# Kernel tuning notes

Measured on AMD Instinct MI355X. Metric: run time of the kernel, lower is better.

The kernel has to match this reference:

```python
import jax, jax.numpy as jnp
import numpy as np


def _bilinear_resize_nchw(x, out_h, out_w):
    """Torch F.interpolate(mode='bilinear', align_corners=False), no antialias."""
    B, C, H, W = x.shape

    def coords(out_n, in_n):
        src = jnp.maximum(0.0, (jnp.arange(out_n, dtype=jnp.float32) + 0.5) * (in_n / out_n) - 0.5)
        f = jnp.floor(src)
        i0 = jnp.clip(f.astype(jnp.int32), 0, in_n - 1)
        i1 = jnp.clip(i0 + 1, 0, in_n - 1)
        frac = src - f
        return i0, i1, frac

    y0, y1, fy = coords(out_h, H)
    x0, x1, fx = coords(out_w, W)
    rows = x[:, :, y0, :] * (1.0 - fy)[None, None, :, None] + x[:, :, y1, :] * fy[None, None, :, None]
    out = rows[:, :, :, x0] * (1.0 - fx)[None, None, None, :] + rows[:, :, :, x1] * fx[None, None, None, :]
    return out


def setup_inputs() -> dict:
    key = jax.random.key(0)
    k1, k2, k3, k4 = jax.random.split(key, 4)
    return {
        "query_value": jax.random.normal(k1, (2, 256, 64, 128), dtype=jnp.float32),
        "memory_keys_low": jax.random.normal(k2, (2, 4, 64, 32, 64), dtype=jnp.float32),
        "memory_values_low": jax.random.normal(k3, (2, 4, 256, 32, 64), dtype=jnp.float32),
        "query_key_low": jax.random.normal(k4, (2, 64, 32, 64), dtype=jnp.float32),
    }


def reference(query_value, memory_keys_low, memory_values_low, query_key_low):
    B, T, Ck, H, W = memory_keys_low.shape
    Cv = memory_values_low.shape[2]
    # keys: BxTxCkxHxW -> Bx(T*H*W)xCk via permute(0,2,1,3,4)+view+permute
    mk = jnp.transpose(memory_keys_low, (0, 2, 1, 3, 4)).reshape(B, Ck, T * H * W)
    qk = query_key_low.reshape(B, Ck, H * W)
    # attn[b, m, n] over memory locations m (softmax axis), query locations n
    attn = jnp.einsum('bcm,bcn->bmn', mk, qk)  # [B, T*H*W, H*W]
    # matmul_norm=False: no key_channels**-0.5 scaling
    attn = jax.nn.softmax(attn, axis=1)
    mv = jnp.transpose(memory_values_low, (0, 2, 1, 3, 4)).reshape(B, Cv, T * H * W)
    memory = jnp.einsum('bcm,bmn->bcn', mv, attn).reshape(B, Cv, H, W)
    qv = _bilinear_resize_nchw(query_value, H, W)
    return jnp.concatenate([qv, memory], axis=1)  # [B, 2*Cv, H, W]
```

## Files before the change

### kernel.cpp

```cpp
#include <hip/hip_runtime.h>
#include <cstdint>

#define BATCH 2
#define TT    4
#define CKD   64
#define CVD   256
#define NQ    2048
#define MM    8192
#define TQ    64
#define TM    32
#define MSPLIT 8
#define MCHUNK (MM / MSPLIT)
#define NIT    (MCHUNK / TM)

typedef unsigned short u16;
typedef __bf16 bf16x8 __attribute__((ext_vector_type(8)));
typedef float  f32x4  __attribute__((ext_vector_type(4)));

struct __attribute__((aligned(8)))  U16x4 { u16 x, y, z, w; };
struct __attribute__((aligned(16))) U16x8 { u16 v[8]; };

__device__ __forceinline__ u16 f2bf(float x) {
    uint32_t u = __float_as_uint(x);
    uint32_t r = (u + 0x7FFFu + ((u >> 16) & 1u)) >> 16;
    return (u16)r;
}
__device__ __forceinline__ float bf2f(u16 h) {
    return __uint_as_float(((uint32_t)h) << 16);
}

#define MFMA(a, b, c) __builtin_amdgcn_mfma_f32_16x16x32_bf16((a), (b), (c), 0, 0, 0)

#define WS_VB   0u
#define WS_KHI  8388608u
#define WS_KLO  10485760u
#define WS_QHI  12582912u
#define WS_QLO  13107200u
#define WS_LP   13631488u
#define WS_UP   13893632u

__global__ __launch_bounds__(256)
void prep_fused(const float* __restrict__ qv, const float* __restrict__ mk,
                const float* __restrict__ qk, const float* __restrict__ mv,
                float* __restrict__ out, u16* __restrict__ vb,
                u16* __restrict__ khi, u16* __restrict__ klo,
                u16* __restrict__ qhi, u16* __restrict__ qlo) {
    __shared__ float tile[64 * 65];
    const int bid = blockIdx.x;
    const int tid = threadIdx.x;

    if (bid < 4096) {
        int idx = bid * 256 + tid;
        int n  = idx & 2047;
        int bc = idx >> 11;
        int x = n & 63, y = n >> 6;
        const float* ib = qv + (size_t)bc * (64 * 128) + (2 * y) * 128 + 2 * x;
        float2 r0 = *(const float2*)ib;
        float2 r1 = *(const float2*)(ib + 128);
        int b = bc >> 8, c = bc & 255;
        out[((size_t)(b * 512 + c)) * NQ + n] = 0.25f * (r0.x + r0.y + r1.x + r1.y);
    } else if (bid < 6144) {
        int idx = (bid - 4096) * 256 + tid;
        const float4* s = (const float4*)mv + (size_t)idx * 2;
        float4 a = s[0], b = s[1];
        U16x8 o;
        o.v[0] = f2bf(a.x); o.v[1] = f2bf(a.y); o.v[2] = f2bf(a.z); o.v[3] = f2bf(a.w);
        o.v[4] = f2bf(b.x); o.v[5] = f2bf(b.y); o.v[6] = f2bf(b.z); o.v[7] = f2bf(b.w);
        *(U16x8*)(vb + (size_t)idx * 8) = o;
    } else {
        const float* src;
        u16 *dhi, *dlo;
        int blk;
        if (bid < 6400) { src = mk; dhi = khi; dlo = klo; blk = bid - 6144; }
        else            { src = qk; dhi = qhi; dlo = qlo; blk = bid - 6400; }
        const int g  = blk >> 5;
        const int mg = blk & 31;
        const float* s = src + (size_t)g * 64 * 2048 + mg * 64;

        const int c = tid >> 2;
        const int q = tid & 3;
        #pragma unroll
        for (int i = 0; i < 4; ++i) {
            float4 v = *(const float4*)(s + (size_t)c * 2048 + q * 16 + i * 4);
            int m = q * 16 + i * 4;
            tile[(m + 0) * 65 + c] = v.x;
            tile[(m + 1) * 65 + c] = v.y;
            tile[(m + 2) * 65 + c] = v.z;
            tile[(m + 3) * 65 + c] = v.w;
        }
        __syncthreads();

        const int mo = tid >> 2;
        const int cb = (tid & 3) * 16;
        U16x8 h0, h1, l0, l1;
        #pragma unroll
        for (int j = 0; j < 8; ++j) {
            float v = tile[mo * 65 + cb + j];
            u16 h = f2bf(v);
            h0.v[j] = h; l0.v[j] = f2bf(v - bf2f(h));
            float v2 = tile[mo * 65 + cb + 8 + j];
            u16 h2 = f2bf(v2);
            h1.v[j] = h2; l1.v[j] = f2bf(v2 - bf2f(h2));
        }
        size_t o = ((size_t)g * 2048 + mg * 64 + mo) * 64 + cb;
        *(U16x8*)(dhi + o) = h0; *(U16x8*)(dhi + o + 8) = h1;
        *(U16x8*)(dlo + o) = l0; *(U16x8*)(dlo + o + 8) = l1;
    }
}

__global__ __launch_bounds__(256, 2)
void flash_attn(const u16* __restrict__ khi_g, const u16* __restrict__ klo_g,
                const u16* __restrict__ vb_g, const u16* __restrict__ qhi_g,
                const u16* __restrict__ qlo_g, float* __restrict__ Up,
                float* __restrict__ Lp) {
    __shared__ __align__(16) u16 smem[2][7168];

    const int tid    = threadIdx.x;
    const int bx     = blockIdx.x;
    const int mchunk = bx & 7;
    const int ntile  = (bx >> 3) & 31;
    const int b      = bx >> 8;

    const int lane = tid & 63;
    const int w    = tid >> 6;
    const int quad = lane >> 4;
    const int l15  = lane & 15;

    const int bt      = b * TT + (mchunk >> 1);
    const int hw_base = (mchunk & 1) * MCHUNK;

    bf16x8 qh[2][2], ql[2][2];
    {
        const int nbase = ntile * TQ + (w >> 1) * 32;
        #pragma unroll
        for (int nsi = 0; nsi < 2; ++nsi) {
            size_t o = ((size_t)(b * NQ + nbase + nsi * 16 + l15)) * 64 + quad * 8;
            qh[nsi][0] = *(const bf16x8*)&qhi_g[o];
            qh[nsi][1] = *(const bf16x8*)&qhi_g[o + 32];
            ql[nsi][0] = *(const bf16x8*)&qlo_g[o];
            ql[nsi][1] = *(const bf16x8*)&qlo_g[o + 32];
        }
    }

    const u16* kh_base = khi_g + ((size_t)bt * 2048 + hw_base) * 64;
    const u16* kl_base = klo_g + ((size_t)bt * 2048 + hw_base) * 64;
    const u16* v_frag_base = vb_g + (size_t)bt * CVD * 2048 + hw_base
                           + (size_t)(w * 64 + l15) * 2048 + quad * 8;

    f32x4 O[4][4];
    #pragma unroll
    for (int i = 0; i < 4; ++i)
        #pragma unroll
        for (int j = 0; j < 4; ++j)
            O[i][j] = (f32x4){0.f, 0.f, 0.f, 0.f};
    float Lloc[2] = {0.f, 0.f};

    const int msub     = w & 1;
    const int nsubpair = w >> 1;

    const int km = tid >> 3;
    const int kc = (tid & 7) * 8;

    bf16x8 kh_r = *(const bf16x8*)&kh_base[(size_t)km * 64 + kc];
    bf16x8 kl_r = *(const bf16x8*)&kl_base[(size_t)km * 64 + kc];
    bf16x8 v_cur[4], v_next[4];
    #pragma unroll
    for (int cs = 0; cs < 4; ++cs)
        v_cur[cs] = *(const bf16x8*)&v_frag_base[(size_t)(cs * 16) * 2048];

    #pragma unroll 2
    for (int it = 0; it < NIT; ++it) {
        u16* Khi = smem[it & 1];
        u16* Klo = Khi + 2304;
        u16* Ps  = Khi + 4608;

        *(bf16x8*)&Khi[km * 72 + kc] = kh_r;
        *(bf16x8*)&Klo[km * 72 + kc] = kl_r;
        __syncthreads();

        f32x4 acc[2];
        acc[0] = (f32x4){0.f, 0.f, 0.f, 0.f};
        acc[1] = (f32x4){0.f, 0.f, 0.f, 0.f};
        #pragma unroll
        for (int ks = 0; ks < 2; ++ks) {
            bf16x8 ah = *(const bf16x8*)&Khi[(msub * 16 + l15) * 72 + ks * 32 + quad * 8];
            bf16x8 al = *(const bf16x8*)&Klo[(msub * 16 + l15) * 72 + ks * 32 + quad * 8];
            #pragma unroll
            for (int nsi = 0; nsi < 2; ++nsi) {
                acc[nsi] = MFMA(ah, qh[nsi][ks], acc[nsi]);
                acc[nsi] = MFMA(ah, ql[nsi][ks], acc[nsi]);
                acc[nsi] = MFMA(al, qh[nsi][ks], acc[nsi]);
            }
        }
        #pragma unroll
        for (int nsi = 0; nsi < 2; ++nsi) {
            int n = (nsubpair * 2 + nsi) * 16 + l15;
            float p0 = __expf(acc[nsi][0]);
            float p1 = __expf(acc[nsi][1]);
            float p2 = __expf(acc[nsi][2]);
            float p3 = __expf(acc[nsi][3]);
            Lloc[nsi] += (p0 + p1) + (p2 + p3);
            U16x4 pk = {f2bf(p0), f2bf(p1), f2bf(p2), f2bf(p3)};
            *(U16x4*)&Ps[n * 40 + msub * 16 + quad * 4] = pk;
        }
        __syncthreads();

        if (it + 1 < NIT) {
            const int hw1 = (it + 1) * TM;
            kh_r = *(const bf16x8*)&kh_base[(size_t)(hw1 + km) * 64 + kc];
            kl_r = *(const bf16x8*)&kl_base[(size_t)(hw1 + km) * 64 + kc];
            #pragma unroll
            for (int cs = 0; cs < 4; ++cs)
                v_next[cs] = *(const bf16x8*)&v_frag_base[(size_t)(cs * 16) * 2048 + hw1];
        }

        bf16x8 a2[4];
        #pragma unroll
        for (int nsub = 0; nsub < 4; ++nsub)
            a2[nsub] = *(const bf16x8*)&Ps[(nsub * 16 + l15) * 40 + quad * 8];
        #pragma unroll
        for (int cs = 0; cs < 4; ++cs)
            #pragma unroll
            for (int nsub = 0; nsub < 4; ++nsub)
                O[nsub][cs] = MFMA(a2[nsub], v_cur[cs], O[nsub][cs]);

        #pragma unroll
        for (int cs = 0; cs < 4; ++cs)
            v_cur[cs] = v_next[cs];
    }

    #pragma unroll
    for (int nsi = 0; nsi < 2; ++nsi) {
        float v = Lloc[nsi];
        v += __shfl_xor(v, 16);
        v += __shfl_xor(v, 32);
        if (quad == nsi) {
            int nsub = nsubpair * 2 + nsi;
            Lp[(((size_t)mchunk * 2 + msub) * BATCH + b) * NQ + ntile * TQ + nsub * 16 + l15] = v;
        }
    }

    float* ubase = Up + (((size_t)mchunk * BATCH + b) * NQ + ntile * TQ) * CVD + w * 64;
    #pragma unroll
    for (int nsub = 0; nsub < 4; ++nsub) {
        #pragma unroll
        for (int cs = 0; cs < 4; ++cs) {
            #pragma unroll
            for (int r = 0; r < 4; ++r) {
                int n_local = nsub * 16 + quad * 4 + r;
                ubase[(size_t)n_local * CVD + cs * 16 + l15] = O[nsub][cs][r];
            }
        }
    }
}

__global__ __launch_bounds__(256) void reduce_div(const float* __restrict__ Up,
                                                  const float* __restrict__ Lp,
                                                  float* __restrict__ out) {
    __shared__ float lds[16 * 65];
    const int tid = threadIdx.x;
    const int cq  = blockIdx.x & 3;
    const int n0  = ((blockIdx.x >> 2) & 127) * 16;
    const int b   = blockIdx.x >> 9;

    const int n_local = tid >> 4;
    const int c_loc   = (tid & 15) * 4;
    const int c       = cq * 64 + c_loc;

    float4 acc = {0.f, 0.f, 0.f, 0.f};
    for (int ms = 0; ms < MSPLIT; ++ms) {
        float4 v = *(const float4*)(Up + (((size_t)ms * BATCH + b) * NQ + n0 + n_local) * CVD + c);
        acc.x += v.x; acc.y += v.y; acc.z += v.z; acc.w += v.w;
    }

    float Lsum = 0.f;
    #pragma unroll
    for (int s = 0; s < MSPLIT * 2; ++s)
        Lsum += Lp[((size_t)s * BATCH + b) * NQ + n0 + n_local];
    const float inv = 1.0f / Lsum;

    lds[n_local * 65 + c_loc + 0] = acc.x * inv;
    lds[n_local * 65 + c_loc + 1] = acc.y * inv;
    lds[n_local * 65 + c_loc + 2] = acc.z * inv;
    lds[n_local * 65 + c_loc + 3] = acc.w * inv;
    __syncthreads();

    const int c_out = tid >> 2;
    const int nq    = (tid & 3) * 4;
    float4 v;
    v.x = lds[(nq + 0) * 65 + c_out];
    v.y = lds[(nq + 1) * 65 + c_out];
    v.z = lds[(nq + 2) * 65 + c_out];
    v.w = lds[(nq + 3) * 65 + c_out];
    *(float4*)(out + ((size_t)(b * 512 + 256 + cq * 64 + c_out)) * NQ + n0 + nq) = v;
}

extern "C" void kernel_launch(void* const* d_in, const int* in_sizes, int n_in,
                              void* d_out, int out_size, void* d_ws, size_t ws_size,
                              hipStream_t stream) {
    const float* qv = (const float*)d_in[0];
    const float* mk = (const float*)d_in[1];
    const float* mv = (const float*)d_in[2];
    const float* qk = (const float*)d_in[3];
    float* out = (float*)d_out;

    u16*   vb  = (u16*)((char*)d_ws + WS_VB);
    u16*   khi = (u16*)((char*)d_ws + WS_KHI);
    u16*   klo = (u16*)((char*)d_ws + WS_KLO);
    u16*   qhi = (u16*)((char*)d_ws + WS_QHI);
    u16*   qlo = (u16*)((char*)d_ws + WS_QLO);
    float* Lp  = (float*)((char*)d_ws + WS_LP);
    float* Up  = (float*)((char*)d_ws + WS_UP);

    prep_fused<<<6464, 256, 0, stream>>>(qv, mk, qk, mv, out, vb, khi, klo, qhi, qlo);
    flash_attn<<<512, 256, 0, stream>>>(khi, klo, vb, qhi, qlo, Up, Lp);
    reduce_div<<<1024, 256, 0, stream>>>(Up, Lp, out);
}
```

Before: 134.6 us.

## Double the memory tile to 64 and give each wave a full query slice

```diff
diff --git a/kernel.cpp b/kernel.cpp
--- a/kernel.cpp
+++ b/kernel.cpp
@@ -8,7 +8,7 @@
 #define NQ    2048
 #define MM    8192
 #define TQ    64
-#define TM    32
+#define TM    64
 #define MSPLIT 8
 #define MCHUNK (MM / MSPLIT)
 #define NIT    (MCHUNK / TM)
@@ -113,7 +113,7 @@
                 const u16* __restrict__ vb_g, const u16* __restrict__ qhi_g,
                 const u16* __restrict__ qlo_g, float* __restrict__ Up,
                 float* __restrict__ Lp) {
-    __shared__ __align__(16) u16 smem[2][7168];
+    __shared__ __align__(16) u16 smem[2][13824];
 
     const int tid    = threadIdx.x;
     const int bx     = blockIdx.x;
@@ -129,17 +129,13 @@
     const int bt      = b * TT + (mchunk >> 1);
     const int hw_base = (mchunk & 1) * MCHUNK;
 
-    bf16x8 qh[2][2], ql[2][2];
+    bf16x8 qh[2], ql[2];
     {
-        const int nbase = ntile * TQ + (w >> 1) * 32;
-        #pragma unroll
-        for (int nsi = 0; nsi < 2; ++nsi) {
-            size_t o = ((size_t)(b * NQ + nbase + nsi * 16 + l15)) * 64 + quad * 8;
-            qh[nsi][0] = *(const bf16x8*)&qhi_g[o];
-            qh[nsi][1] = *(const bf16x8*)&qhi_g[o + 32];
-            ql[nsi][0] = *(const bf16x8*)&qlo_g[o];
-            ql[nsi][1] = *(const bf16x8*)&qlo_g[o + 32];
-        }
+        size_t o = ((size_t)(b * NQ + ntile * TQ + w * 16 + l15)) * 64 + quad * 8;
+        qh[0] = *(const bf16x8*)&qhi_g[o];
+        qh[1] = *(const bf16x8*)&qhi_g[o + 32];
+        ql[0] = *(const bf16x8*)&qlo_g[o];
+        ql[1] = *(const bf16x8*)&qlo_g[o + 32];
     }
 
     const u16* kh_base = khi_g + ((size_t)bt * 2048 + hw_base) * 64;
@@ -153,91 +149,98 @@
         #pragma unroll
         for (int j = 0; j < 4; ++j)
             O[i][j] = (f32x4){0.f, 0.f, 0.f, 0.f};
-    float Lloc[2] = {0.f, 0.f};
-
-    const int msub     = w & 1;
-    const int nsubpair = w >> 1;
-
-    const int km = tid >> 3;
-    const int kc = (tid & 7) * 8;
-
-    bf16x8 kh_r = *(const bf16x8*)&kh_base[(size_t)km * 64 + kc];
-    bf16x8 kl_r = *(const bf16x8*)&kl_base[(size_t)km * 64 + kc];
-    bf16x8 v_cur[4], v_next[4];
+    float Lloc = 0.f;
+
+    const int km = tid >> 2;
+    const int kc = (tid & 3) * 16;
+
+    bf16x8 kh_r0 = *(const bf16x8*)&kh_base[(size_t)km * 64 + kc];
+    bf16x8 kh_r1 = *(const bf16x8*)&kh_base[(size_t)km * 64 + kc + 8];
+    bf16x8 kl_r0 = *(const bf16x8*)&kl_base[(size_t)km * 64 + kc];
+    bf16x8 kl_r1 = *(const bf16x8*)&kl_base[(size_t)km * 64 + kc + 8];
+    bf16x8 v_cur[4][2], v_next[4][2];
     #pragma unroll
     for (int cs = 0; cs < 4; ++cs)
-        v_cur[cs] = *(const bf16x8*)&v_frag_base[(size_t)(cs * 16) * 2048];
+        #pragma unroll
+        for (int ks = 0; ks < 2; ++ks)
+            v_cur[cs][ks] = *(const bf16x8*)&v_frag_base[(size_t)(cs * 16) * 2048 + ks * 32];
 
     #pragma unroll 2
     for (int it = 0; it < NIT; ++it) {
         u16* Khi = smem[it & 1];
-        u16* Klo = Khi + 2304;
-        u16* Ps  = Khi + 4608;
-
-        *(bf16x8*)&Khi[km * 72 + kc] = kh_r;
-        *(bf16x8*)&Klo[km * 72 + kc] = kl_r;
+        u16* Klo = Khi + 4608;
+        u16* Ps  = Khi + 9216;
+
+        *(bf16x8*)&Khi[km * 72 + kc]     = kh_r0;
+        *(bf16x8*)&Khi[km * 72 + kc + 8] = kh_r1;
+        *(bf16x8*)&Klo[km * 72 + kc]     = kl_r0;
+        *(bf16x8*)&Klo[km * 72 + kc + 8] = kl_r1;
         __syncthreads();
 
-        f32x4 acc[2];
-        acc[0] = (f32x4){0.f, 0.f, 0.f, 0.f};
-        acc[1] = (f32x4){0.f, 0.f, 0.f, 0.f};
+        f32x4 acc[4];
+        #pragma unroll
+        for (int ms = 0; ms < 4; ++ms)
+            acc[ms] = (f32x4){0.f, 0.f, 0.f, 0.f};
         #pragma unroll
         for (int ks = 0; ks < 2; ++ks) {
-            bf16x8 ah = *(const bf16x8*)&Khi[(msub * 16 + l15) * 72 + ks * 32 + quad * 8];
-            bf16x8 al = *(const bf16x8*)&Klo[(msub * 16 + l15) * 72 + ks * 32 + quad * 8];
             #pragma unroll
-            for (int nsi = 0; nsi < 2; ++nsi) {
-                acc[nsi] = MFMA(ah, qh[nsi][ks], acc[nsi]);
-                acc[nsi] = MFMA(ah, ql[nsi][ks], acc[nsi]);
-                acc[nsi] = MFMA(al, qh[nsi][ks], acc[nsi]);
+            for (int ms = 0; ms < 4; ++ms) {
+                bf16x8 ah = *(const bf16x8*)&Khi[(ms * 16 + l15) * 72 + ks * 32 + quad * 8];
+                bf16x8 al = *(const bf16x8*)&Klo[(ms * 16 + l15) * 72 + ks * 32 + quad * 8];
+                acc[ms] = MFMA(ah, qh[ks], acc[ms]);
+                acc[ms] = MFMA(ah, ql[ks], acc[ms]);
+                acc[ms] = MFMA(al, qh[ks], acc[ms]);
             }
         }
         #pragma unroll
-        for (int nsi = 0; nsi < 2; ++nsi) {
-            int n = (nsubpair * 2 + nsi) * 16 + l15;
-            float p0 = __expf(acc[nsi][0]);
-            float p1 = __expf(acc[nsi][1]);
-            float p2 = __expf(acc[nsi][2]);
-            float p3 = __expf(acc[nsi][3]);
-            Lloc[nsi] += (p0 + p1) + (p2 + p3);
+        for (int ms = 0; ms < 4; ++ms) {
+            float p0 = __expf(acc[ms][0]);
+            float p1 = __expf(acc[ms][1]);
+            float p2 = __expf(acc[ms][2]);
+            float p3 = __expf(acc[ms][3]);
+            Lloc += (p0 + p1) + (p2 + p3);
             U16x4 pk = {f2bf(p0), f2bf(p1), f2bf(p2), f2bf(p3)};
-            *(U16x4*)&Ps[n * 40 + msub * 16 + quad * 4] = pk;
+            *(U16x4*)&Ps[(w * 16 + l15) * 72 + ms * 16 + quad * 4] = pk;
         }
         __syncthreads();
 
         if (it + 1 < NIT) {
             const int hw1 = (it + 1) * TM;
-            kh_r = *(const bf16x8*)&kh_base[(size_t)(hw1 + km) * 64 + kc];
-            kl_r = *(const bf16x8*)&kl_base[(size_t)(hw1 + km) * 64 + kc];
+            kh_r0 = *(const bf16x8*)&kh_base[(size_t)(hw1 + km) * 64 + kc];
+            kh_r1 = *(const bf16x8*)&kh_base[(size_t)(hw1 + km) * 64 + kc + 8];
+            kl_r0 = *(const bf16x8*)&kl_base[(size_t)(hw1 + km) * 64 + kc];
+            kl_r1 = *(const bf16x8*)&kl_base[(size_t)(hw1 + km) * 64 + kc + 8];
             #pragma unroll
             for (int cs = 0; cs < 4; ++cs)
-                v_next[cs] = *(const bf16x8*)&v_frag_base[(size_t)(cs * 16) * 2048 + hw1];
-        }
-
-        bf16x8 a2[4];
-        #pragma unroll
-        for (int nsub = 0; nsub < 4; ++nsub)
-            a2[nsub] = *(const bf16x8*)&Ps[(nsub * 16 + l15) * 40 + quad * 8];
-        #pragma unroll
-        for (int cs = 0; cs < 4; ++cs)
+                #pragma unroll
+                for (int ks = 0; ks < 2; ++ks)
+                    v_next[cs][ks] = *(const bf16x8*)&v_frag_base[(size_t)(cs * 16) * 2048 + ks * 32 + hw1];
+        }
+
+        #pragma unroll
+        for (int ks = 0; ks < 2; ++ks) {
             #pragma unroll
-            for (int nsub = 0; nsub < 4; ++nsub)
-                O[nsub][cs] = MFMA(a2[nsub], v_cur[cs], O[nsub][cs]);
-
-        #pragma unroll
-        for (int cs = 0; cs < 4; ++cs)
-            v_cur[cs] = v_next[cs];
-    }
-
-    #pragma unroll
-    for (int nsi = 0; nsi < 2; ++nsi) {
-        float v = Lloc[nsi];
+            for (int nsub = 0; nsub < 4; ++nsub) {
+                bf16x8 a2 = *(const bf16x8*)&Ps[(nsub * 16 + l15) * 72 + ks * 32 + quad * 8];
+                #pragma unroll
+                for (int cs = 0; cs < 4; ++cs)
+                    O[nsub][cs] = MFMA(a2, v_cur[cs][ks], O[nsub][cs]);
+            }
+        }
+
+        #pragma unroll
+        for (int cs = 0; cs < 4; ++cs) {
+            v_cur[cs][0] = v_next[cs][0];
+            v_cur[cs][1] = v_next[cs][1];
+        }
+    }
+
+    {
+        float v = Lloc;
         v += __shfl_xor(v, 16);
         v += __shfl_xor(v, 32);
-        if (quad == nsi) {
-            int nsub = nsubpair * 2 + nsi;
-            Lp[(((size_t)mchunk * 2 + msub) * BATCH + b) * NQ + ntile * TQ + nsub * 16 + l15] = v;
-        }
+        if (quad == 0)
+            Lp[((size_t)mchunk * BATCH + b) * NQ + ntile * TQ + w * 16 + l15] = v;
     }
 
     float* ubase = Up + (((size_t)mchunk * BATCH + b) * NQ + ntile * TQ) * CVD + w * 64;
@@ -275,8 +278,8 @@
 
     float Lsum = 0.f;
     #pragma unroll
-    for (int s = 0; s < MSPLIT * 2; ++s)
-        Lsum += Lp[((size_t)s * BATCH + b) * NQ + n0 + n_local];
+    for (int ms = 0; ms < MSPLIT; ++ms)
+        Lsum += Lp[((size_t)ms * BATCH + b) * NQ + n0 + n_local];
     const float inv = 1.0f / Lsum;
 
     lds[n_local * 65 + c_loc + 0] = acc.x * inv;
```

After: 143.6 us. +6.7%, slower.

## Load K fragments directly from global into registers, drop K LDS staging

Applied to the files above, without the earlier changes.

```diff
diff --git a/kernel.cpp b/kernel.cpp
--- a/kernel.cpp
+++ b/kernel.cpp
@@ -71,8 +71,10 @@
         const float* src;
         u16 *dhi, *dlo;
         int blk;
-        if (bid < 6400) { src = mk; dhi = khi; dlo = klo; blk = bid - 6144; }
-        else            { src = qk; dhi = qhi; dlo = qlo; blk = bid - 6400; }
+        float scale;
+        if (bid < 6400) { src = mk; dhi = khi; dlo = klo; blk = bid - 6144; scale = 1.0f; }
+        else            { src = qk; dhi = qhi; dlo = qlo; blk = bid - 6400;
+                          scale = 1.4426950408889634f; }
         const int g  = blk >> 5;
         const int mg = blk & 31;
         const float* s = src + (size_t)g * 64 * 2048 + mg * 64;
@@ -95,10 +97,10 @@
         U16x8 h0, h1, l0, l1;
         #pragma unroll
         for (int j = 0; j < 8; ++j) {
-            float v = tile[mo * 65 + cb + j];
+            float v = tile[mo * 65 + cb + j] * scale;
             u16 h = f2bf(v);
             h0.v[j] = h; l0.v[j] = f2bf(v - bf2f(h));
-            float v2 = tile[mo * 65 + cb + 8 + j];
+            float v2 = tile[mo * 65 + cb + 8 + j] * scale;
             u16 h2 = f2bf(v2);
             h1.v[j] = h2; l1.v[j] = f2bf(v2 - bf2f(h2));
         }
@@ -113,7 +115,7 @@
                 const u16* __restrict__ vb_g, const u16* __restrict__ qhi_g,
                 const u16* __restrict__ qlo_g, float* __restrict__ Up,
                 float* __restrict__ Lp) {
-    __shared__ __align__(16) u16 smem[2][7168];
+    __shared__ __align__(16) u16 Ps2[2][2560];
 
     const int tid    = threadIdx.x;
     const int bx     = blockIdx.x;
@@ -129,9 +131,12 @@
     const int bt      = b * TT + (mchunk >> 1);
     const int hw_base = (mchunk & 1) * MCHUNK;
 
+    const int msub     = w & 1;
+    const int nsubpair = w >> 1;
+
     bf16x8 qh[2][2], ql[2][2];
     {
-        const int nbase = ntile * TQ + (w >> 1) * 32;
+        const int nbase = ntile * TQ + nsubpair * 32;
         #pragma unroll
         for (int nsi = 0; nsi < 2; ++nsi) {
             size_t o = ((size_t)(b * NQ + nbase + nsi * 16 + l15)) * 64 + quad * 8;
@@ -144,6 +149,7 @@
 
     const u16* kh_base = khi_g + ((size_t)bt * 2048 + hw_base) * 64;
     const u16* kl_base = klo_g + ((size_t)bt * 2048 + hw_base) * 64;
+    const size_t k_off = (size_t)(msub * 16 + l15) * 64 + quad * 8;
     const u16* v_frag_base = vb_g + (size_t)bt * CVD * 2048 + hw_base
                            + (size_t)(w * 64 + l15) * 2048 + quad * 8;
 
@@ -155,65 +161,61 @@
             O[i][j] = (f32x4){0.f, 0.f, 0.f, 0.f};
     float Lloc[2] = {0.f, 0.f};
 
-    const int msub     = w & 1;
-    const int nsubpair = w >> 1;
-
-    const int km = tid >> 3;
-    const int kc = (tid & 7) * 8;
-
-    bf16x8 kh_r = *(const bf16x8*)&kh_base[(size_t)km * 64 + kc];
-    bf16x8 kl_r = *(const bf16x8*)&kl_base[(size_t)km * 64 + kc];
-    bf16x8 v_cur[4], v_next[4];
+    bf16x8 kh[2][2], kl[2][2], vv[2][4];
+    #pragma unroll
+    for (int ks = 0; ks < 2; ++ks) {
+        kh[0][ks] = *(const bf16x8*)&kh_base[k_off + ks * 32];
+        kl[0][ks] = *(const bf16x8*)&kl_base[k_off + ks * 32];
+    }
     #pragma unroll
     for (int cs = 0; cs < 4; ++cs)
-        v_cur[cs] = *(const bf16x8*)&v_frag_base[(size_t)(cs * 16) * 2048];
+        vv[0][cs] = *(const bf16x8*)&v_frag_base[(size_t)(cs * 16) * 2048];
 
     #pragma unroll 2
     for (int it = 0; it < NIT; ++it) {
-        u16* Khi = smem[it & 1];
-        u16* Klo = Khi + 2304;
-        u16* Ps  = Khi + 4608;
-
-        *(bf16x8*)&Khi[km * 72 + kc] = kh_r;
-        *(bf16x8*)&Klo[km * 72 + kc] = kl_r;
-        __syncthreads();
-
-        f32x4 acc[2];
-        acc[0] = (f32x4){0.f, 0.f, 0.f, 0.f};
-        acc[1] = (f32x4){0.f, 0.f, 0.f, 0.f};
+        const int p = it & 1;
+        u16* Ps = Ps2[p];
+
+        if (it + 1 < NIT) {
+            const size_t row64 = (size_t)(it + 1) * TM * 64;
+            const int hw1 = (it + 1) * TM;
+            #pragma unroll
+            for (int ks = 0; ks < 2; ++ks) {
+                kh[p ^ 1][ks] = *(const bf16x8*)&kh_base[row64 + k_off + ks * 32];
+                kl[p ^ 1][ks] = *(const bf16x8*)&kl_base[row64 + k_off + ks * 32];
+            }
+            #pragma unroll
+            for (int cs = 0; cs < 4; ++cs)
+                vv[p ^ 1][cs] = *(const bf16x8*)&v_frag_base[(size_t)(cs * 16) * 2048 + hw1];
+        }
+
+        f32x4 acch[2], accl[2];
+        acch[0] = (f32x4){0.f, 0.f, 0.f, 0.f};
+        acch[1] = (f32x4){0.f, 0.f, 0.f, 0.f};
+        accl[0] = (f32x4){0.f, 0.f, 0.f, 0.f};
+        accl[1] = (f32x4){0.f, 0.f, 0.f, 0.f};
         #pragma unroll
         for (int ks = 0; ks < 2; ++ks) {
-            bf16x8 ah = *(const bf16x8*)&Khi[(msub * 16 + l15) * 72 + ks * 32 + quad * 8];
-            bf16x8 al = *(const bf16x8*)&Klo[(msub * 16 + l15) * 72 + ks * 32 + quad * 8];
             #pragma unroll
             for (int nsi = 0; nsi < 2; ++nsi) {
-                acc[nsi] = MFMA(ah, qh[nsi][ks], acc[nsi]);
-                acc[nsi] = MFMA(ah, ql[nsi][ks], acc[nsi]);
-                acc[nsi] = MFMA(al, qh[nsi][ks], acc[nsi]);
+                acch[nsi] = MFMA(kh[p][ks], qh[nsi][ks], acch[nsi]);
+                accl[nsi] = MFMA(kh[p][ks], ql[nsi][ks], accl[nsi]);
+                accl[nsi] = MFMA(kl[p][ks], qh[nsi][ks], accl[nsi]);
             }
         }
         #pragma unroll
         for (int nsi = 0; nsi < 2; ++nsi) {
             int n = (nsubpair * 2 + nsi) * 16 + l15;
-            float p0 = __expf(acc[nsi][0]);
-            float p1 = __expf(acc[nsi][1]);
-            float p2 = __expf(acc[nsi][2]);
-            float p3 = __expf(acc[nsi][3]);
+            float p0 = exp2f(acch[nsi][0] + accl[nsi][0]);
+            float p1 = exp2f(acch[nsi][1] + accl[nsi][1]);
+            float p2 = exp2f(acch[nsi][2] + accl[nsi][2]);
+            float p3 = exp2f(acch[nsi][3] + accl[nsi][3]);
             Lloc[nsi] += (p0 + p1) + (p2 + p3);
             U16x4 pk = {f2bf(p0), f2bf(p1), f2bf(p2), f2bf(p3)};
             *(U16x4*)&Ps[n * 40 + msub * 16 + quad * 4] = pk;
         }
         __syncthreads();
 
-        if (it + 1 < NIT) {
-            const int hw1 = (it + 1) * TM;
-            kh_r = *(const bf16x8*)&kh_base[(size_t)(hw1 + km) * 64 + kc];
-            kl_r = *(const bf16x8*)&kl_base[(size_t)(hw1 + km) * 64 + kc];
-            #pragma unroll
-            for (int cs = 0; cs < 4; ++cs)
-                v_next[cs] = *(const bf16x8*)&v_frag_base[(size_t)(cs * 16) * 2048 + hw1];
-        }
-
         bf16x8 a2[4];
         #pragma unroll
         for (int nsub = 0; nsub < 4; ++nsub)
@@ -222,11 +224,7 @@
         for (int cs = 0; cs < 4; ++cs)
             #pragma unroll
             for (int nsub = 0; nsub < 4; ++nsub)
-                O[nsub][cs] = MFMA(a2[nsub], v_cur[cs], O[nsub][cs]);
-
-        #pragma unroll
-        for (int cs = 0; cs < 4; ++cs)
-            v_cur[cs] = v_next[cs];
+                O[nsub][cs] = MFMA(a2[nsub], vv[p][cs], O[nsub][cs]);
     }
 
     #pragma unroll
```

After: 159.4 us. 18.4% more time.
